# Kernel optimization log

Measured on AMD Instinct MI355X. Metric: run time of the kernel, lower is better.

The kernel has to match this reference:

```python
import jax, jax.numpy as jnp
import numpy as np

B, C, H, W, D, V = 1, 32, 128, 160, 48, 3


def _make_proj_matrices():
    # K @ [R|t] per view, small rotations/baselines so warps land mostly in-bounds
    K = np.array([[400.0, 0.0, 80.0], [0.0, 400.0, 64.0], [0.0, 0.0, 1.0]])
    mats = []
    for v in range(V):
        a = 0.04 * v
        R = np.array([[np.cos(a), 0.0, np.sin(a)], [0.0, 1.0, 0.0], [-np.sin(a), 0.0, np.cos(a)]])
        t = np.array([120.0 * v, 0.0, 0.0])  # baseline in mm, consistent with depth ~425..935
        P = np.eye(4)
        P[:3, :3] = K @ R
        P[:3, 3] = K @ t
        mats.append(P)
    return jnp.asarray(np.stack(mats)[None], dtype=jnp.float32)  # [1,V,4,4]


def setup_inputs() -> dict:
    key = jax.random.key(0)
    k0, k1, k2, kw = jax.random.split(key, 4)
    feat0 = jax.random.normal(k0, (B, C, H, W), jnp.float32)
    feat1 = jax.random.normal(k1, (B, C, H, W), jnp.float32)
    feat2 = jax.random.normal(k2, (B, C, H, W), jnp.float32)
    depth_values = jnp.broadcast_to(
        jnp.linspace(425.0, 935.0, D, dtype=jnp.float32)[None], (B, D))
    w_reg = jax.random.normal(kw, (1, C, 3, 3, 3), jnp.float32) * 0.05
    b_reg = jnp.zeros((1,), jnp.float32)
    return dict(feat0=feat0, feat1=feat1, feat2=feat2,
                proj_matrices=_make_proj_matrices(),
                depth_values=depth_values, w_reg=w_reg, b_reg=b_reg,
                num_depth=D)


def _bilinear_sample(fea, gx, gy):
    # fea: [C,H,W]; gx,gy: [N] pixel coords (align_corners=True convention),
    # zero padding outside image (matches F.grid_sample padding_mode='zeros').
    h, w = fea.shape[1], fea.shape[2]
    x0 = jnp.floor(gx)
    y0 = jnp.floor(gy)
    wx = gx - x0
    wy = gy - y0

    def corner(xi, yi, wgt):
        valid = ((xi >= 0) & (xi <= w - 1) & (yi >= 0) & (yi <= h - 1)).astype(fea.dtype)
        xc = jnp.clip(xi, 0, w - 1).astype(jnp.int32)
        yc = jnp.clip(yi, 0, h - 1).astype(jnp.int32)
        return fea[:, yc, xc] * (wgt * valid)[None]  # [C,N]

    return (corner(x0, y0, (1 - wx) * (1 - wy)) +
            corner(x0 + 1, y0, wx * (1 - wy)) +
            corner(x0, y0 + 1, (1 - wx) * wy) +
            corner(x0 + 1, y0 + 1, wx * wy))


def homo_warping(src_fea, src_proj, ref_proj, depth_values):
    # src_fea [B,C,H,W], projs [B,4,4], depth_values [B,D] -> [B,C,D,H,W]
    b, c, h, w = src_fea.shape
    d = depth_values.shape[1]
    proj = src_proj @ jnp.linalg.inv(ref_proj)
    rot = proj[:, :3, :3]           # [B,3,3]
    trans = proj[:, :3, 3]          # [B,3]
    yy, xx = jnp.meshgrid(jnp.arange(h, dtype=src_fea.dtype),
                          jnp.arange(w, dtype=src_fea.dtype), indexing='ij')
    xyz = jnp.stack([xx.ravel(), yy.ravel(), jnp.ones(h * w, src_fea.dtype)], 0)  # [3,HW]
    rot_xyz = jnp.einsum('bij,jn->bin', rot, xyz)                                  # [B,3,HW]
    p = rot_xyz[:, :, None, :] * depth_values[:, None, :, None] + trans[:, :, None, None]  # [B,3,D,HW]
    z = p[:, 2]
    gx = (p[:, 0] / z).reshape(b, -1)  # [B, D*HW]
    gy = (p[:, 1] / z).reshape(b, -1)
    warped = jax.vmap(_bilinear_sample)(src_fea, gx, gy)  # [B,C,D*HW]
    return warped.reshape(b, c, d, h, w)


def reference(feat0, feat1, feat2, proj_matrices, depth_values, w_reg, b_reg, num_depth):
    features = [feat0, feat1, feat2]
    projs = [proj_matrices[:, v] for v in range(proj_matrices.shape[1])]
    ref_fea, ref_proj = features[0], projs[0]
    num_views = len(features)
    b, c, h, w = ref_fea.shape

    ref_volume = jnp.broadcast_to(ref_fea[:, :, None], (b, c, num_depth, h, w))
    volume_sum = ref_volume
    volume_sq_sum = ref_volume ** 2
    for src_fea, src_proj in zip(features[1:], projs[1:]):
        wv = homo_warping(src_fea, src_proj, ref_proj, depth_values)
        volume_sum = volume_sum + wv
        volume_sq_sum = volume_sq_sum + wv * wv

    volume_variance = volume_sq_sum / num_views - (volume_sum / num_views) ** 2

    # cost_regularization stand-in: 3D conv C -> 1, SAME padding, then squeeze channel
    cost = jax.lax.conv_general_dilated(
        volume_variance, w_reg, window_strides=(1, 1, 1), padding='SAME',
        dimension_numbers=('NCDHW', 'OIDHW', 'NCDHW'))
    cost = cost[:, 0] + b_reg[0]            # [B,D,H,W]

    prob_volume = jax.nn.softmax(cost, axis=1)
    depth = jnp.sum(prob_volume * depth_values[:, :, None, None], axis=1)  # [B,H,W]
    photometric_confidence = jnp.max(prob_volume, axis=1)                   # [B,H,W]
    return depth, photometric_confidence
```

## Files before the change

### kernel.cpp

```cpp
#include <hip/hip_runtime.h>
#include <hip/hip_fp16.h>
#include <math.h>

#define Cc 32
#define Hc 128
#define Wc 160
#define Dc 48
#define HWc (Hc*Wc)
#define TSX 16
#define TSY 8
#define HALOX (TSX+2)
#define HALOY (TSY+2)
#define NPOS (HALOX*HALOY)
#define DCHUNK 6
#define NCHUNK (Dc/DCHUNK)
#define NPASS 3
#define NSLOT (DCHUNK+2)


typedef _Float16 h8v __attribute__((ext_vector_type(8)));
typedef float f32x4 __attribute__((ext_vector_type(4)));

union F4H { float4 f; __half2 h[4]; };
union PackCW { __half2 h[4]; float4 f; };
union AF { float4 f; h8v h; };

__global__ void k_pre(const float* __restrict__ f0, const float* __restrict__ f1,
                      const float* __restrict__ f2, const float* __restrict__ proj,
                      const float* __restrict__ wreg,
                      _Float16* __restrict__ o0, _Float16* __restrict__ o1, _Float16* __restrict__ o2,
                      float* __restrict__ wsproj, _Float16* __restrict__ w2h,
                      float* __restrict__ costvol) {
    const int tid = threadIdx.x;
    const int p = blockIdx.x * 256 + tid;
    if (blockIdx.y == 3) {
        if (p < HWc) {
#pragma unroll
            for (int d = 0; d < Dc; d++) costvol[d * HWc + p] = 0.f;
        }
        return;
    }
    if (p < HWc) {
        const float* f = (blockIdx.y == 0) ? f0 : (blockIdx.y == 1) ? f1 : f2;
        _Float16*    o = (blockIdx.y == 0) ? o0 : (blockIdx.y == 1) ? o1 : o2;
        float v[Cc];
#pragma unroll
        for (int c = 0; c < Cc; c++) v[c] = f[c * HWc + p];
        union { __half2 h[16]; float4 f4[4]; } rec;
#pragma unroll
        for (int c = 0; c < 16; c++) rec.h[c] = __floats2half2_rn(v[2 * c], v[2 * c + 1]);
        float4* o4 = (float4*)(o + (size_t)p * Cc);
#pragma unroll
        for (int j = 0; j < 4; j++) o4[j] = rec.f4[j];
    }
    if (blockIdx.x == 0 && blockIdx.y == 0) {
        for (int i = tid; i < 9 * 3 * Cc; i += 256) {
            int ch = i & 31;
            int t  = i >> 5;
            int kd = t % 3;
            int khkw = t / 3;
            w2h[i] = (_Float16)wreg[ch * 27 + kd * 9 + khkw];
        }
        if (tid == 0) {
            float a[4][8];
            for (int i = 0; i < 4; i++)
                for (int j = 0; j < 4; j++) {
                    a[i][j]     = proj[i * 4 + j];
                    a[i][j + 4] = (i == j) ? 1.f : 0.f;
                }
            for (int col = 0; col < 4; col++) {
                int piv = col; float best = fabsf(a[col][col]);
                for (int r = col + 1; r < 4; r++) {
                    float v = fabsf(a[r][col]);
                    if (v > best) { best = v; piv = r; }
                }
                if (piv != col)
                    for (int j = 0; j < 8; j++) { float t = a[col][j]; a[col][j] = a[piv][j]; a[piv][j] = t; }
                float inv = 1.f / a[col][col];
                for (int j = 0; j < 8; j++) a[col][j] *= inv;
                for (int r = 0; r < 4; r++) if (r != col) {
                    float f = a[r][col];
                    for (int j = 0; j < 8; j++) a[r][j] -= f * a[col][j];
                }
            }
            for (int v = 1; v < 3; v++) {
                const float* P = proj + v * 16;
                float M[3][4];
                for (int i = 0; i < 3; i++)
                    for (int j = 0; j < 4; j++) {
                        float s = 0.f;
                        for (int k = 0; k < 4; k++) s += P[i * 4 + k] * a[k][4 + j];
                        M[i][j] = s;
                    }
                float* o = wsproj + (v - 1) * 12;
                o[0] = M[0][0]; o[1] = M[0][1]; o[2] = M[0][2];
                o[3] = M[1][0]; o[4] = M[1][1]; o[5] = M[1][2];
                o[6] = M[2][0]; o[7] = M[2][1]; o[8] = M[2][2];
                o[9] = M[0][3]; o[10] = M[1][3]; o[11] = M[2][3];
            }
        }
    }
}

__global__ __launch_bounds__(256, 4) void k_cost(
    const _Float16* __restrict__ fT0, const _Float16* __restrict__ fT1,
    const _Float16* __restrict__ fT2, const float* __restrict__ dvals,
    const float4* __restrict__ w2h4, const float* __restrict__ wsproj,
    float* __restrict__ costvol)
{
    __shared__ float4 varA[NPOS * 4];
    __shared__ float4 varB[NPOS * 4];
    __shared__ float4 parW[NPOS];
    __shared__ uint2  parIc[NPOS];
    __shared__ float4 cost_l4[NSLOT * 32];
    __shared__ float projl[24];
    float* cost_l = (float*)cost_l4;

    const int tid = threadIdx.x;
    if (tid < 24) projl[tid] = wsproj[tid];
#pragma unroll
    for (int i = 0; i < 4; i++) cost_l[i * 256 + tid] = 0.f;
    __syncthreads();

    const int tileX = blockIdx.x;
    const int sy    = blockIdx.y;
    const int d0    = blockIdx.z * DCHUNK;
    const int baseH = sy * TSY - 1, baseW = tileX * TSX - 1;

    const int posq = tid >> 2;
    const int cc   = tid & 3;

    const int wid  = tid >> 6;
    const int lane = tid & 63;
    const int lrow = lane & 15;
    const int lsel = lane >> 4;

    const float4* fT0_4 = (const float4*)fT0;
    const float4* fT1_4 = (const float4*)fT1;
    const float4* fT2_4 = (const float4*)fT2;

    h8v bfr[9];
    {
        const int kdc = (lrow < 3) ? lrow : 0;
#pragma unroll
        for (int t = 0; t < 9; t++) {
            AF u; u.f = w2h4[(t * 3 + kdc) * 4 + lsel];
            bfr[t] = u.h;
        }
    }

    float rAx[2], rAy[2], rAz[2];
    float trn[2][3];
#pragma unroll
    for (int v = 0; v < 2; v++) {
        trn[v][0] = projl[v * 12 + 9];
        trn[v][1] = projl[v * 12 + 10];
        trn[v][2] = projl[v * 12 + 11];
    }
    bool aok;
    {
        int pp = (tid < NPOS) ? tid : 0;
        int py = pp / HALOX, px = pp % HALOX;
        int hyi = baseH + py, hxi = baseW + px;
        aok = (tid < NPOS) && hyi >= 0 && hyi < Hc && hxi >= 0 && hxi < Wc;
        float hx = (float)hxi, hy = (float)hyi;
#pragma unroll
        for (int v = 0; v < 2; v++) {
            const float* R = projl + v * 12;
            rAx[v] = fmaf(R[0], hx, fmaf(R[1], hy, R[2]));
            rAy[v] = fmaf(R[3], hx, fmaf(R[4], hy, R[5]));
            rAz[v] = fmaf(R[6], hx, fmaf(R[7], hy, R[8]));
        }
    }

    int    bmask = 0;
    float4 rfv[NPASS];
#pragma unroll
    for (int s = 0; s < NPASS; s++) {
        int p = posq + s * 64;
        bool act = p < NPOS;
        int pp = act ? p : 0;
        int py = pp / HALOX, px = pp % HALOX;
        int hyi = baseH + py, hxi = baseW + px;
        bool ok = act && hyi >= 0 && hyi < Hc && hxi >= 0 && hxi < Wc;
        if (ok) bmask |= (1 << s);
        rfv[s] = ok ? fT0_4[(hyi * Wc + hxi) * 4 + cc] : make_float4(0.f, 0.f, 0.f, 0.f);
    }

    auto phaseA = [&](int dpn) {
        const float depthN = dvals[dpn];
        if (aok) {
            float cw[2][4]; unsigned int pkc[2];
#pragma unroll
            for (int v = 0; v < 2; v++) {
                float X = fmaf(rAx[v], depthN, trn[v][0]);
                float Y = fmaf(rAy[v], depthN, trn[v][1]);
                float Z = fmaf(rAz[v], depthN, trn[v][2]);
                float iz = 1.f / Z;
                float gx = X * iz, gy = Y * iz;
                float x0f = floorf(gx), y0f = floorf(gy);
                float wx = gx - x0f, wy = gy - y0f;
                int x0 = (int)x0f, y0 = (int)y0f;
                bool vx0 = (x0 >= 0) & (x0 <= Wc - 1);
                bool vx1 = (x0 + 1 >= 0) & (x0 + 1 <= Wc - 1);
                bool vy0 = (y0 >= 0) & (y0 <= Hc - 1);
                bool vy1 = (y0 + 1 >= 0) & (y0 + 1 <= Hc - 1);
                unsigned int xc0 = (unsigned int)min(max(x0, 0), Wc - 1);
                unsigned int xc1 = (unsigned int)min(max(x0 + 1, 0), Wc - 1);
                unsigned int yc0 = (unsigned int)min(max(y0, 0), Hc - 1);
                unsigned int yc1 = (unsigned int)min(max(y0 + 1, 0), Hc - 1);
                float ax = 1.f - wx, ay = 1.f - wy;
                cw[v][0] = (vx0 && vy0) ? ax * ay : 0.f;
                cw[v][1] = (vx1 && vy0) ? wx * ay : 0.f;
                cw[v][2] = (vx0 && vy1) ? ax * wy : 0.f;
                cw[v][3] = (vx1 && vy1) ? wx * wy : 0.f;
                pkc[v] = xc0 | (xc1 << 8) | (yc0 << 16) | (yc1 << 24);
            }
            PackCW pc;
            pc.h[0] = __floats2half2_rn(cw[0][0], cw[0][1]);
            pc.h[1] = __floats2half2_rn(cw[0][2], cw[0][3]);
            pc.h[2] = __floats2half2_rn(cw[1][0], cw[1][1]);
            pc.h[3] = __floats2half2_rn(cw[1][2], cw[1][3]);
            parW[tid] = pc.f;
            parIc[tid] = make_uint2(pkc[0], pkc[1]);
        }
    };

    const __half2 kT3 = __float2half2_rn(1.f / 3.f);
    const __half2 kN9 = __float2half2_rn(-1.f / 9.f);

    auto phaseB = [&](float4* dst) {
#pragma unroll
        for (int s = 0; s < NPASS; s++) {
            int p = posq + s * 64;
            if (p >= NPOS) continue;
            const int vaddr = (p << 2) + (cc ^ ((p >> 1) & 3));
            if (!((bmask >> s) & 1)) {
                dst[vaddr] = make_float4(0.f, 0.f, 0.f, 0.f);
                continue;
            }
            PackCW pc; pc.f = parW[p];
            uint2 pi = parIc[p];
            __half2 c0a = __low2half2(pc.h[0]), c0b = __high2half2(pc.h[0]);
            __half2 c0c = __low2half2(pc.h[1]), c0d = __high2half2(pc.h[1]);
            __half2 c1a = __low2half2(pc.h[2]), c1b = __high2half2(pc.h[2]);
            __half2 c1c = __low2half2(pc.h[3]), c1d = __high2half2(pc.h[3]);
            unsigned int a = pi.x, b = pi.y;
            int x00 = a & 0xff, x01 = (a >> 8) & 0xff, y00 = (a >> 16) & 0xff, y01 = a >> 24;
            int x10 = b & 0xff, x11 = (b >> 8) & 0xff, y10 = (b >> 16) & 0xff, y11 = b >> 24;
            int i00 = y00 * Wc + x00, i01 = y00 * Wc + x01;
            int i02 = y01 * Wc + x00, i03 = y01 * Wc + x01;
            int i10 = y10 * Wc + x10, i11 = y10 * Wc + x11;
            int i12 = y11 * Wc + x10, i13 = y11 * Wc + x11;
            F4H rf; rf.f = rfv[s];
            F4H t00, t01, t10, t11, u00v, u01v, u10v, u11v, vo;
            t00.f = fT1_4[i00 * 4 + cc];
            t01.f = fT1_4[i01 * 4 + cc];
            t10.f = fT1_4[i02 * 4 + cc];
            t11.f = fT1_4[i03 * 4 + cc];
            u00v.f = fT2_4[i10 * 4 + cc];
            u01v.f = fT2_4[i11 * 4 + cc];
            u10v.f = fT2_4[i12 * 4 + cc];
            u11v.f = fT2_4[i13 * 4 + cc];
#pragma unroll
            for (int j = 0; j < 4; j++) {
                __half2 a1 = __hfma2(c0a, t00.h[j], __hfma2(c0b, t01.h[j],
                             __hfma2(c0c, t10.h[j], __hmul2(c0d, t11.h[j]))));
                __half2 a2 = __hfma2(c1a, u00v.h[j], __hfma2(c1b, u01v.h[j],
                             __hfma2(c1c, u10v.h[j], __hmul2(c1d, u11v.h[j]))));
                __half2 r  = rf.h[j];
                __half2 sm = __hadd2(r, __hadd2(a1, a2));
                __half2 sq = __hfma2(r, r, __hfma2(a1, a1, __hmul2(a2, a2)));
                vo.h[j] = __hfma2(__hmul2(sm, sm), kN9, __hmul2(sq, kT3));
            }
            dst[vaddr] = vo.f;
        }
    };

    auto conv = [&](const float4* src, int dp) {
#pragma unroll
        for (int g = 0; g < 2; g++) {
            const int R = (wid << 1) + g;
            f32x4 acc = {0.f, 0.f, 0.f, 0.f};
#pragma unroll
            for (int t = 0; t < 9; t++) {
                const int dy = t / 3, dx = t % 3;
                const int pos = (R + dy) * HALOX + dx + lrow;
                AF a; a.f = src[(pos << 2) + (lsel ^ ((pos >> 1) & 3))];
                acc = __builtin_amdgcn_mfma_f32_16x16x32_f16(a.h, bfr[t], acc, 0, 0, 0);
            }
            if (lrow < 3) {
                const int idx = ((dp - d0) + 2 - lrow) * 32 + R * 4 + lsel;
                float4 c = cost_l4[idx];
                c.x += acc[0]; c.y += acc[1]; c.z += acc[2]; c.w += acc[3];
                cost_l4[idx] = c;
            }
        }
    };

    const int dpLast = d0 + DCHUNK - 1;

    phaseA(d0);
    __syncthreads();
    phaseB(varA);
    __syncthreads();
    phaseA(d0 + 1);
    __syncthreads();

    for (int i = 0; i < DCHUNK / 2; i++) {
        const int t = d0 + 2 * i;
        phaseB(varB);
        conv(varA, t);
        __syncthreads();
        if (t + 2 <= dpLast) {
            phaseA(t + 2);
            __syncthreads();
        }
        if (t + 2 <= dpLast) phaseB(varA);
        conv(varB, t + 1);
        __syncthreads();
        if (t + 3 <= dpLast) {
            phaseA(t + 3);
            __syncthreads();
        }
    }

    const int c    = tid & 127;
    const int half = tid >> 7;
    const int gy = sy * TSY + (c >> 4), gx = tileX * TSX + (c & 15);
    float* cbase = costvol + gy * Wc + gx;
#pragma unroll
    for (int k = 0; k < 4; k++) {
        const int slot = half * 4 + k;
        const int s = d0 + slot - 1;
        if (s >= 0 && s < Dc)
            atomicAdd(cbase + (size_t)s * HWc, cost_l[slot * 128 + c]);
    }
}

__global__ void k_softmax(const float* __restrict__ costvol, const float* __restrict__ dvals,
                          const float* __restrict__ breg, float* __restrict__ out)
{
    const int px = blockIdx.x * 256 + threadIdx.x;
    if (px >= HWc) return;
    const float bias = breg[0];
    float c[Dc];
    float m = -1e30f;
#pragma unroll
    for (int d = 0; d < Dc; d++) {
        c[d] = costvol[d * HWc + px] + bias;
        m = fmaxf(m, c[d]);
    }
    float se = 0.f, sed = 0.f, me = 0.f;
#pragma unroll
    for (int d = 0; d < Dc; d++) {
        float e = __expf(c[d] - m);
        se += e;
        sed = fmaf(e, dvals[d], sed);
        me = fmaxf(me, e);
    }
    float inv = 1.f / se;
    out[px]       = sed * inv;
    out[HWc + px] = me * inv;
}

extern "C" void kernel_launch(void* const* d_in, const int* in_sizes, int n_in,
                              void* d_out, int out_size, void* d_ws, size_t ws_size,
                              hipStream_t stream) {
    const float* f0    = (const float*)d_in[0];
    const float* f1    = (const float*)d_in[1];
    const float* f2    = (const float*)d_in[2];
    const float* proj  = (const float*)d_in[3];
    const float* dvals = (const float*)d_in[4];
    const float* wreg  = (const float*)d_in[5];
    const float* breg  = (const float*)d_in[6];

    float* ws      = (float*)d_ws;
    float* wsproj  = ws;
    _Float16* w2h  = (_Float16*)(ws + 32);
    _Float16* fT0h = (_Float16*)(ws + 32 + 432);
    _Float16* fT1h = fT0h + (size_t)HWc * Cc;
    _Float16* fT2h = fT1h + (size_t)HWc * Cc;
    float* costvol = (float*)(fT2h + (size_t)HWc * Cc);

    k_pre<<<dim3((HWc + 255) / 256, 4), 256, 0, stream>>>(f0, f1, f2, proj, wreg,
                                                          fT0h, fT1h, fT2h, wsproj, w2h,
                                                          costvol);

    dim3 grid(Wc / TSX, Hc / TSY, NCHUNK);
    k_cost<<<grid, 256, 0, stream>>>(fT0h, fT1h, fT2h, dvals, (const float4*)w2h,
                                     wsproj, costvol);

    k_softmax<<<(HWc + 255) / 256, 256, 0, stream>>>(costvol, dvals, breg, (float*)d_out);
}
```

Measured before the change: 119.1 us.

## Replace cost-volume atomics with direct stores plus boundary buffers, split softmax over depth

The cost kernel now writes its interior depth slices directly and sends halo slices that overlap neighbouring chunks into a separate boundary buffer, so atomicAdd and the zero-fill pass over the cost volume are no longer needed. The softmax kernel adds the boundary contributions back, splits the 48 depths across four thread groups, and merges partial max and sum values through shared memory. The pre-kernel is also split across two thread halves per pixel to give more threads. This costs extra workspace and a more intricate index mapping that must line up exactly with the chunk halo layout.

```diff
diff --git a/kernel.cpp b/kernel.cpp
--- a/kernel.cpp
+++ b/kernel.cpp
@@ -29,29 +29,22 @@
                       const float* __restrict__ f2, const float* __restrict__ proj,
                       const float* __restrict__ wreg,
                       _Float16* __restrict__ o0, _Float16* __restrict__ o1, _Float16* __restrict__ o2,
-                      float* __restrict__ wsproj, _Float16* __restrict__ w2h,
-                      float* __restrict__ costvol) {
+                      float* __restrict__ wsproj, _Float16* __restrict__ w2h) {
     const int tid = threadIdx.x;
-    const int p = blockIdx.x * 256 + tid;
-    if (blockIdx.y == 3) {
-        if (p < HWc) {
-#pragma unroll
-            for (int d = 0; d < Dc; d++) costvol[d * HWc + p] = 0.f;
-        }
-        return;
-    }
-    if (p < HWc) {
+    const int pxl = tid & 127, h = tid >> 7;
+    const int p = blockIdx.x * 128 + pxl;
+    {
         const float* f = (blockIdx.y == 0) ? f0 : (blockIdx.y == 1) ? f1 : f2;
         _Float16*    o = (blockIdx.y == 0) ? o0 : (blockIdx.y == 1) ? o1 : o2;
-        float v[Cc];
-#pragma unroll
-        for (int c = 0; c < Cc; c++) v[c] = f[c * HWc + p];
-        union { __half2 h[16]; float4 f4[4]; } rec;
-#pragma unroll
-        for (int c = 0; c < 16; c++) rec.h[c] = __floats2half2_rn(v[2 * c], v[2 * c + 1]);
+        float v[16];
+#pragma unroll
+        for (int c = 0; c < 16; c++) v[c] = f[(h * 16 + c) * HWc + p];
+        union { __half2 hh[8]; float4 f4[2]; } rec;
+#pragma unroll
+        for (int c = 0; c < 8; c++) rec.hh[c] = __floats2half2_rn(v[2 * c], v[2 * c + 1]);
         float4* o4 = (float4*)(o + (size_t)p * Cc);
-#pragma unroll
-        for (int j = 0; j < 4; j++) o4[j] = rec.f4[j];
+        o4[h * 2 + 0] = rec.f4[0];
+        o4[h * 2 + 1] = rec.f4[1];
     }
     if (blockIdx.x == 0 && blockIdx.y == 0) {
         for (int i = tid; i < 9 * 3 * Cc; i += 256) {
@@ -106,7 +99,7 @@
     const _Float16* __restrict__ fT0, const _Float16* __restrict__ fT1,
     const _Float16* __restrict__ fT2, const float* __restrict__ dvals,
     const float4* __restrict__ w2h4, const float* __restrict__ wsproj,
-    float* __restrict__ costvol)
+    float* __restrict__ costvol, float* __restrict__ bnd)
 {
     __shared__ float4 varA[NPOS * 4];
     __shared__ float4 varB[NPOS * 4];
@@ -124,7 +117,8 @@
 
     const int tileX = blockIdx.x;
     const int sy    = blockIdx.y;
-    const int d0    = blockIdx.z * DCHUNK;
+    const int zc    = blockIdx.z;
+    const int d0    = zc * DCHUNK;
     const int baseH = sy * TSY - 1, baseW = tileX * TSX - 1;
 
     const int posq = tid >> 2;
@@ -328,40 +322,68 @@
     const int c    = tid & 127;
     const int half = tid >> 7;
     const int gy = sy * TSY + (c >> 4), gx = tileX * TSX + (c & 15);
-    float* cbase = costvol + gy * Wc + gx;
+    const int gpx = gy * Wc + gx;
 #pragma unroll
     for (int k = 0; k < 4; k++) {
         const int slot = half * 4 + k;
-        const int s = d0 + slot - 1;
-        if (s >= 0 && s < Dc)
-            atomicAdd(cbase + (size_t)s * HWc, cost_l[slot * 128 + c]);
+        const float v = cost_l[slot * 128 + c];
+        if (slot == 0) {
+            if (zc > 0) bnd[(zc * 2 + 0) * HWc + gpx] = v;
+        } else if (slot == NSLOT - 1) {
+            if (zc < NCHUNK - 1) bnd[(zc * 2 + 1) * HWc + gpx] = v;
+        } else {
+            costvol[(size_t)(d0 + slot - 1) * HWc + gpx] = v;
+        }
     }
 }
 
-__global__ void k_softmax(const float* __restrict__ costvol, const float* __restrict__ dvals,
+__global__ void k_softmax(const float* __restrict__ costvol, const float* __restrict__ bnd,
+                          const float* __restrict__ dvals,
                           const float* __restrict__ breg, float* __restrict__ out)
 {
-    const int px = blockIdx.x * 256 + threadIdx.x;
-    if (px >= HWc) return;
+    __shared__ float sm[4][64], ss[4][64], sd[4][64], sx[4][64];
+    const int tid = threadIdx.x;
+    const int pxl = tid & 63, g = tid >> 6;
+    const int px = blockIdx.x * 64 + pxl;
     const float bias = breg[0];
-    float c[Dc];
+
+    float c[12];
     float m = -1e30f;
 #pragma unroll
-    for (int d = 0; d < Dc; d++) {
-        c[d] = costvol[d * HWc + px] + bias;
-        m = fmaxf(m, c[d]);
+    for (int i = 0; i < 12; i++) {
+        const int d = g * 12 + i;
+        float v = costvol[(size_t)d * HWc + px] + bias;
+        if (i == 0) { if (g > 0) v += bnd[(4 * g - 1) * HWc + px]; }
+        if (i == 6) v += bnd[(4 * g + 1) * HWc + px];
+        if (i == 5) v += bnd[(4 * g + 2) * HWc + px];
+        if (i == 11) { if (g < 3) v += bnd[(4 * g + 4) * HWc + px]; }
+        c[i] = v;
+        m = fmaxf(m, v);
     }
     float se = 0.f, sed = 0.f, me = 0.f;
 #pragma unroll
-    for (int d = 0; d < Dc; d++) {
-        float e = __expf(c[d] - m);
+    for (int i = 0; i < 12; i++) {
+        float e = __expf(c[i] - m);
         se += e;
-        sed = fmaf(e, dvals[d], sed);
+        sed = fmaf(e, dvals[g * 12 + i], sed);
         me = fmaxf(me, e);
     }
-    float inv = 1.f / se;
-    out[px]       = sed * inv;
-    out[HWc + px] = me * inv;
+    sm[g][pxl] = m; ss[g][pxl] = se; sd[g][pxl] = sed; sx[g][pxl] = me;
+    __syncthreads();
+    if (g == 0) {
+        float M = fmaxf(fmaxf(sm[0][pxl], sm[1][pxl]), fmaxf(sm[2][pxl], sm[3][pxl]));
+        float SE = 0.f, SD = 0.f, ME = 0.f;
+#pragma unroll
+        for (int j = 0; j < 4; j++) {
+            float w = __expf(sm[j][pxl] - M);
+            SE += ss[j][pxl] * w;
+            SD += sd[j][pxl] * w;
+            ME = fmaxf(ME, sx[j][pxl] * w);
+        }
+        float inv = 1.f / SE;
+        out[px]       = SD * inv;
+        out[HWc + px] = ME * inv;
+    }
 }
 
 extern "C" void kernel_launch(void* const* d_in, const int* in_sizes, int n_in,
@@ -382,14 +404,14 @@
     _Float16* fT1h = fT0h + (size_t)HWc * Cc;
     _Float16* fT2h = fT1h + (size_t)HWc * Cc;
     float* costvol = (float*)(fT2h + (size_t)HWc * Cc);
-
-    k_pre<<<dim3((HWc + 255) / 256, 4), 256, 0, stream>>>(f0, f1, f2, proj, wreg,
-                                                          fT0h, fT1h, fT2h, wsproj, w2h,
-                                                          costvol);
+    float* bnd     = costvol + (size_t)Dc * HWc;
+
+    k_pre<<<dim3(HWc / 128, 3), 256, 0, stream>>>(f0, f1, f2, proj, wreg,
+                                                  fT0h, fT1h, fT2h, wsproj, w2h);
 
     dim3 grid(Wc / TSX, Hc / TSY, NCHUNK);
     k_cost<<<grid, 256, 0, stream>>>(fT0h, fT1h, fT2h, dvals, (const float4*)w2h,
-                                     wsproj, costvol);
-
-    k_softmax<<<(HWc + 255) / 256, 256, 0, stream>>>(costvol, dvals, breg, (float*)d_out);
+                                     wsproj, costvol, bnd);
+
+    k_softmax<<<HWc / 64, 256, 0, stream>>>(costvol, bnd, dvals, breg, (float*)d_out);
 }
```

Result: no change. 119.2 us (+0.1%).
